# Performance work log

Hardware: AMD Instinct MI355X
Metric: run time of the kernel (lower is better)

## Reference

```python
import jax, jax.numpy as jnp
import numpy as np

HEADS = 16
DIM_HEAD = 64
QUERY_DIM = 1024
INNER_DIM = HEADS * DIM_HEAD  # 1024
SCALE = DIM_HEAD ** -0.5


def setup_inputs() -> dict:
    key = jax.random.key(0)
    ks = jax.random.split(key, 6)
    B, S = 2, 2048
    hidden_states = jax.random.normal(ks[0], (B, S, QUERY_DIM), dtype=jnp.float32)
    # torch Linear weights are [out, in]; store transposed [in, out] for x @ W
    w_q = jax.random.normal(ks[1], (QUERY_DIM, INNER_DIM), dtype=jnp.float32) * (QUERY_DIM ** -0.5)
    w_k = jax.random.normal(ks[2], (QUERY_DIM, INNER_DIM), dtype=jnp.float32) * (QUERY_DIM ** -0.5)
    w_v = jax.random.normal(ks[3], (QUERY_DIM, INNER_DIM), dtype=jnp.float32) * (QUERY_DIM ** -0.5)
    w_o = jax.random.normal(ks[4], (INNER_DIM, QUERY_DIM), dtype=jnp.float32) * (INNER_DIM ** -0.5)
    b_o = jax.random.normal(ks[5], (QUERY_DIM,), dtype=jnp.float32) * 0.01
    return {"hidden_states": hidden_states, "w_q": w_q, "w_k": w_k, "w_v": w_v, "w_o": w_o, "b_o": b_o}


def reference(hidden_states, w_q, w_k, w_v, w_o, b_o):
    B, S, _ = hidden_states.shape
    # QKV projections (context = hidden_states, i.e. self-attention)
    q = (hidden_states @ w_q).reshape(B, S, HEADS, DIM_HEAD)
    k = (hidden_states @ w_k).reshape(B, S, HEADS, DIM_HEAD)
    v = (hidden_states @ w_v).reshape(B, S, HEADS, DIM_HEAD)
    # scaled dot-product attention; scores materialized as [B, H, S, S]
    scores = jnp.einsum("bqhd,bkhd->bhqk", q, k) * SCALE
    probs = jax.nn.softmax(scores, axis=-1)
    out = jnp.einsum("bhqk,bkhd->bqhd", probs, v).reshape(B, S, INNER_DIM)
    return out @ w_o + b_o
```

## Files before the change

### kernel.cpp

```cpp
#include <hip/hip_runtime.h>
#include <cstdint>
#include <cstddef>

typedef unsigned short u16;
typedef unsigned int u32;
typedef __bf16 bf16x8 __attribute__((ext_vector_type(8)));
typedef float f32x4 __attribute__((ext_vector_type(4)));
typedef float f32x16 __attribute__((ext_vector_type(16)));
typedef u32 u32x2 __attribute__((ext_vector_type(2)));
typedef u32 u32x4 __attribute__((ext_vector_type(4)));

#define AS1 __attribute__((address_space(1)))
#define AS3 __attribute__((address_space(3)))

__device__ __forceinline__ void gld16(const u16* g, u16* l) {
  __builtin_amdgcn_global_load_lds((const AS1 void*)(const void*)g,
                                   (AS3 void*)(void*)l, 16, 0, 0);
}

__device__ __forceinline__ u16 f2bf(float f) {
  union { float f; unsigned u; } x; x.f = f;
  return (u16)((x.u + 0x7fffu + ((x.u >> 16) & 1u)) >> 16);
}

__device__ __forceinline__ float bf2f(u16 u) {
  union { u32 i; float f; } x; x.i = ((u32)u) << 16; return x.f;
}

__device__ __forceinline__ float fexp2(float x) {
  float r; asm("v_exp_f32 %0, %1" : "=v"(r) : "v"(x)); return r;
}

__device__ __forceinline__ f32x16 zf16() {
  f32x16 v;
#pragma unroll
  for (int i = 0; i < 16; ++i) v[i] = 0.f;
  return v;
}

__device__ __forceinline__ bf16x8 mk8(u32x2 a, u32x2 b) {
  union { u32x4 u; bf16x8 v; } x;
  x.u[0] = a[0]; x.u[1] = a[1]; x.u[2] = b[0]; x.u[3] = b[1];
  return x.v;
}

__global__ void k_prep(const float* __restrict__ X,
                       const float* __restrict__ wq, const float* __restrict__ wk,
                       const float* __restrict__ wv, const float* __restrict__ wo,
                       u16* __restrict__ Xb, u16* __restrict__ Wqkv, u16* __restrict__ Wot) {
  const int z = blockIdx.z;
  if (z == 4) {
    int bid = blockIdx.y * 32 + blockIdx.x;
    int tid = threadIdx.y * 32 + threadIdx.x;
#pragma unroll
    for (int k = 0; k < 4; ++k) {
      int i = bid * 1024 + k * 256 + tid;
      float4 v = reinterpret_cast<const float4*>(X)[i];
      ushort4 o;
      o.x = f2bf(v.x); o.y = f2bf(v.y); o.z = f2bf(v.z); o.w = f2bf(v.w);
      reinterpret_cast<ushort4*>(Xb)[i] = o;
    }
    return;
  }
  __shared__ float t[32][33];
  const float* in = (z == 0) ? wq : (z == 1) ? wk : (z == 2) ? wv : wo;
  u16* out = (z < 3) ? (Wqkv + (size_t)z * 1048576) : Wot;
  int bx = blockIdx.x * 32, by = blockIdx.y * 32;
  int tx = threadIdx.x, ty = threadIdx.y;
#pragma unroll
  for (int j = 0; j < 32; j += 8)
    t[ty + j][tx] = in[(size_t)(by + ty + j) * 1024 + bx + tx];
  __syncthreads();
#pragma unroll
  for (int j = 0; j < 32; j += 8)
    out[(size_t)(bx + ty + j) * 1024 + by + tx] = f2bf(t[tx][ty + j]);
}

__global__ __launch_bounds__(256) void k_gemm_qkv(
    const u16* __restrict__ Xb,
    const u16* __restrict__ Wt,
    u16* __restrict__ Qb,
    u16* __restrict__ Kb,
    u16* __restrict__ Vt) {
  __shared__ __align__(16) u16 As[128][32];
  __shared__ __align__(16) u16 Bs[128][32];
  const int tid = threadIdx.x;
  const int w = tid >> 6, l = tid & 63;
  const int bm = blockIdx.x * 128;
  const int bn = blockIdx.y * 128;
  const int wm = (w >> 1) * 64, wn = (w & 1) * 64;
  const int lm = l & 15, lg = l >> 4;

  f32x4 acc[4][4];
#pragma unroll
  for (int i = 0; i < 4; ++i)
#pragma unroll
    for (int j = 0; j < 4; ++j) acc[i][j] = f32x4{0.f, 0.f, 0.f, 0.f};

  const int srow = w * 16 + (l >> 2);
  const int scol = (l & 3) * 8;
  for (int k0 = 0; k0 < 1024; k0 += 32) {
#pragma unroll
    for (int j = 0; j < 2; ++j) {
      gld16(Xb + (size_t)(bm + j * 64 + srow) * 1024 + k0 + scol, &As[j * 64 + w * 16][0]);
      gld16(Wt + (size_t)(bn + j * 64 + srow) * 1024 + k0 + scol, &Bs[j * 64 + w * 16][0]);
    }
    __syncthreads();
    bf16x8 af[4], bfr[4];
#pragma unroll
    for (int mt = 0; mt < 4; ++mt)
      af[mt] = *reinterpret_cast<const bf16x8*>(&As[wm + mt * 16 + lm][lg * 8]);
#pragma unroll
    for (int nt = 0; nt < 4; ++nt)
      bfr[nt] = *reinterpret_cast<const bf16x8*>(&Bs[wn + nt * 16 + lm][lg * 8]);
#pragma unroll
    for (int mt = 0; mt < 4; ++mt)
#pragma unroll
      for (int nt = 0; nt < 4; ++nt)
        acc[mt][nt] = __builtin_amdgcn_mfma_f32_16x16x32_bf16(af[mt], bfr[nt], acc[mt][nt], 0, 0, 0);
    __syncthreads();
  }
#pragma unroll
  for (int nt = 0; nt < 4; ++nt) {
    int gc = bn + wn + nt * 16 + lm;
    int which = gc >> 10, jc = gc & 1023, h = jc >> 6, d = jc & 63;
#pragma unroll
    for (int mt = 0; mt < 4; ++mt) {
#pragma unroll
      for (int r = 0; r < 4; ++r) {
        int gr = bm + wm + mt * 16 + lg * 4 + r;
        int b = gr >> 11, s = gr & 2047;
        float v = acc[mt][nt][r];
        size_t bh = (size_t)(b * 16 + h);
        if (which == 0)      Qb[(bh * 2048 + s) * 64 + d] = f2bf(v * 0.18033688f);
        else if (which == 1) Kb[(bh * 2048 + s) * 64 + d] = f2bf(v);
        else                 Vt[(bh * 64 + d) * 2048 + s] = f2bf(v);
      }
    }
  }
}

__global__ __launch_bounds__(256) void k_attn(
    const u16* __restrict__ Qb, const u16* __restrict__ Kb,
    const u16* __restrict__ Vt,
    u16* __restrict__ Opb,
    float* __restrict__ lsums) {
  __shared__ __align__(16) u16 Ks[2][4224];
  __shared__ __align__(16) u16 Vs[2][4224];
  const int tid = threadIdx.x, w = tid >> 6, l = tid & 63;
  const int lm = l & 31, hi = l >> 5;
  const int kx = lm & 7;
  const int bh = blockIdx.x;
  const int q0 = blockIdx.y * 128 + w * 32;
  const int z = blockIdx.z;
  const u16* Qh = Qb + (size_t)bh * 2048 * 64;
  const u16* Kh = Kb + ((size_t)bh * 2048 + z * 1024) * 64;
  const u16* Vh = Vt + (size_t)bh * 64 * 2048 + z * 1024;

  bf16x8 qf[4];
#pragma unroll
  for (int c = 0; c < 4; ++c)
    qf[c] = *reinterpret_cast<const bf16x8*>(&Qh[(size_t)(q0 + lm) * 64 + 16 * c + 8 * hi]);

  f32x16 o0 = zf16(), o1 = zf16();
  float lsum = 0.f;

  const int sr8 = l >> 3;
  const int sg = l & 7;
  const int koff = (lm >> 3) * 528 + (lm & 7) * 64;

#define STAGE(tile, buf)                                                          \
  {                                                                               \
    const int kvn_ = (tile) * 64;                                                 \
    _Pragma("unroll")                                                             \
    for (int j = 0; j < 2; ++j) {                                                 \
      int row_ = w * 16 + j * 8 + sr8;                                            \
      int g_ = sg ^ sr8;                                                          \
      gld16(Kh + (size_t)(kvn_ + row_) * 64 + 8 * g_, &Ks[buf][(w * 2 + j) * 528]); \
      gld16(Vh + (size_t)row_ * 2048 + kvn_ + 8 * g_, &Vs[buf][(w * 2 + j) * 528]); \
    }                                                                             \
  }

  STAGE(0, 0);
  __syncthreads();

  for (int t = 0; t < 16; ++t) {
    const int cur = t & 1, nxt = cur ^ 1;

    if (t < 15) STAGE(t + 1, nxt);

    const u16* Kc = &Ks[cur][0];
    bf16x8 pf[2][2];
    float ps0 = 0.f, ps1 = 0.f, ps2 = 0.f, ps3 = 0.f;

    {
      f32x16 st = zf16();
      __builtin_amdgcn_s_setprio(1);
#pragma unroll
      for (int c = 0; c < 4; ++c) {
        bf16x8 kf = *reinterpret_cast<const bf16x8*>(Kc + koff + 8 * ((2 * c + hi) ^ kx));
        st = __builtin_amdgcn_mfma_f32_32x32x16_bf16(kf, qf[c], st, 0, 0, 0);
      }
      __builtin_amdgcn_s_setprio(0);
#pragma unroll
      for (int j = 0; j < 2; ++j)
#pragma unroll
        for (int ii = 0; ii < 8; ++ii) {
          float p = fexp2(st[8 * j + ii]);
          pf[0][j][ii] = (__bf16)p;
          if ((ii & 3) == 0)      ps0 += p;
          else if ((ii & 3) == 1) ps1 += p;
          else if ((ii & 3) == 2) ps2 += p;
          else                    ps3 += p;
        }
    }
    {
      f32x16 st = zf16();
      __builtin_amdgcn_s_setprio(1);
#pragma unroll
      for (int c = 0; c < 4; ++c) {
        bf16x8 kf = *reinterpret_cast<const bf16x8*>(Kc + koff + 2112 + 8 * ((2 * c + hi) ^ kx));
        st = __builtin_amdgcn_mfma_f32_32x32x16_bf16(kf, qf[c], st, 0, 0, 0);
      }
      __builtin_amdgcn_s_setprio(0);
#pragma unroll
      for (int j = 0; j < 2; ++j)
#pragma unroll
        for (int ii = 0; ii < 8; ++ii) {
          float p = fexp2(st[8 * j + ii]);
          pf[1][j][ii] = (__bf16)p;
          if ((ii & 3) == 0)      ps0 += p;
          else if ((ii & 3) == 1) ps1 += p;
          else if ((ii & 3) == 2) ps2 += p;
          else                    ps3 += p;
        }
    }
    float ps = (ps0 + ps1) + (ps2 + ps3);
    ps += __shfl_xor(ps, 32);
    lsum += ps;

    const u16* Vc = &Vs[cur][0];
    __builtin_amdgcn_s_setprio(1);
#pragma unroll
    for (int tt = 0; tt < 2; ++tt)
#pragma unroll
      for (int j = 0; j < 2; ++j) {
        int Ga = 4 * tt + 2 * j;
        u32x2 a0 = *reinterpret_cast<const u32x2*>(Vc + koff + 8 * (Ga ^ kx) + 4 * hi);
        u32x2 a1 = *reinterpret_cast<const u32x2*>(Vc + koff + 8 * ((Ga + 1) ^ kx) + 4 * hi);
        u32x2 b0 = *reinterpret_cast<const u32x2*>(Vc + koff + 2112 + 8 * (Ga ^ kx) + 4 * hi);
        u32x2 b1 = *reinterpret_cast<const u32x2*>(Vc + koff + 2112 + 8 * ((Ga + 1) ^ kx) + 4 * hi);
        o0 = __builtin_amdgcn_mfma_f32_32x32x16_bf16(pf[tt][j], mk8(a0, a1), o0, 0, 0, 0);
        o1 = __builtin_amdgcn_mfma_f32_32x32x16_bf16(pf[tt][j], mk8(b0, b1), o1, 0, 0, 0);
      }
    __builtin_amdgcn_s_setprio(0);

    __syncthreads();
  }
#undef STAGE

  const size_t robase = ((size_t)z * 32 + bh) * 2048 + q0;
  if (!hi) lsums[robase + lm] = lsum;
#pragma unroll
  for (int r = 0; r < 16; ++r) {
    int cr = (r & 3) + 8 * (r >> 2) + 4 * hi;
    size_t ro = (robase + cr) * 64;
    Opb[ro + lm]      = f2bf(o0[r]);
    Opb[ro + 32 + lm] = f2bf(o1[r]);
  }
}

__global__ __launch_bounds__(256) void k_merge(
    const u16* __restrict__ Opb, const float* __restrict__ lsums,
    u16* __restrict__ Ab) {
  int idx = blockIdx.x * 256 + threadIdx.x;
  int d8 = idx & 7, q = (idx >> 3) & 2047, bh = idx >> 14;
  size_t r0 = (size_t)bh * 2048 + q;
  size_t r1 = (size_t)(32 + bh) * 2048 + q;
  float inv = 1.0f / (lsums[r0] + lsums[r1]);
  u32x4 a0 = *reinterpret_cast<const u32x4*>(&Opb[r0 * 64 + d8 * 8]);
  u32x4 a1 = *reinterpret_cast<const u32x4*>(&Opb[r1 * 64 + d8 * 8]);
  u32x4 o;
#pragma unroll
  for (int j = 0; j < 4; ++j) {
    float lo = (bf2f((u16)(a0[j] & 0xffff)) + bf2f((u16)(a1[j] & 0xffff))) * inv;
    float hb = (bf2f((u16)(a0[j] >> 16))    + bf2f((u16)(a1[j] >> 16)))    * inv;
    o[j] = (u32)f2bf(lo) | ((u32)f2bf(hb) << 16);
  }
  int b = bh >> 4, h = bh & 15;
  *reinterpret_cast<u32x4*>(&Ab[((size_t)b * 2048 + q) * 1024 + h * 64 + d8 * 8]) = o;
}

__global__ __launch_bounds__(256) void k_gemm_out(
    const u16* __restrict__ Ab,
    const u16* __restrict__ Wot,
    const float* __restrict__ bias, float* __restrict__ out) {
  __shared__ __align__(16) u16 As[128][32];
  __shared__ __align__(16) u16 Bs[128][32];
  const int tid = threadIdx.x;
  const int w = tid >> 6, l = tid & 63;
  const int bm = blockIdx.x * 128;
  const int bn = blockIdx.y * 128;
  const int wm = (w >> 1) * 64, wn = (w & 1) * 64;
  const int lm = l & 15, lg = l >> 4;

  f32x4 acc[4][4];
#pragma unroll
  for (int i = 0; i < 4; ++i)
#pragma unroll
    for (int j = 0; j < 4; ++j) acc[i][j] = f32x4{0.f, 0.f, 0.f, 0.f};

  const int srow = w * 16 + (l >> 2);
  const int scol = (l & 3) * 8;
  for (int k0 = 0; k0 < 1024; k0 += 32) {
#pragma unroll
    for (int j = 0; j < 2; ++j) {
      gld16(Ab  + (size_t)(bm + j * 64 + srow) * 1024 + k0 + scol, &As[j * 64 + w * 16][0]);
      gld16(Wot + (size_t)(bn + j * 64 + srow) * 1024 + k0 + scol, &Bs[j * 64 + w * 16][0]);
    }
    __syncthreads();
    bf16x8 af[4], bfr[4];
#pragma unroll
    for (int mt = 0; mt < 4; ++mt)
      af[mt] = *reinterpret_cast<const bf16x8*>(&As[wm + mt * 16 + lm][lg * 8]);
#pragma unroll
    for (int nt = 0; nt < 4; ++nt)
      bfr[nt] = *reinterpret_cast<const bf16x8*>(&Bs[wn + nt * 16 + lm][lg * 8]);
#pragma unroll
    for (int mt = 0; mt < 4; ++mt)
#pragma unroll
      for (int nt = 0; nt < 4; ++nt)
        acc[mt][nt] = __builtin_amdgcn_mfma_f32_16x16x32_bf16(af[mt], bfr[nt], acc[mt][nt], 0, 0, 0);
    __syncthreads();
  }
#pragma unroll
  for (int nt = 0; nt < 4; ++nt) {
    int gc = bn + wn + nt * 16 + lm;
    float bv = bias[gc];
#pragma unroll
    for (int mt = 0; mt < 4; ++mt) {
#pragma unroll
      for (int r = 0; r < 4; ++r) {
        int gr = bm + wm + mt * 16 + lg * 4 + r;
        out[(size_t)gr * 1024 + gc] = acc[mt][nt][r] + bv;
      }
    }
  }
}

extern "C" void kernel_launch(void* const* d_in, const int* in_sizes, int n_in,
                              void* d_out, int out_size, void* d_ws, size_t ws_size,
                              hipStream_t stream) {
  const float* X  = (const float*)d_in[0];
  const float* wq = (const float*)d_in[1];
  const float* wk = (const float*)d_in[2];
  const float* wv = (const float*)d_in[3];
  const float* wo = (const float*)d_in[4];
  const float* bo = (const float*)d_in[5];
  float* out = (float*)d_out;

  char* ws = (char*)d_ws;
  u16*   Xb    = (u16*)(ws);
  u16*   Wqkv  = (u16*)(ws + (size_t)(8u  << 20));
  u16*   Wot   = (u16*)(ws + (size_t)(14u << 20));
  u16*   Qb    = (u16*)(ws + (size_t)(16u << 20));
  u16*   Kb    = (u16*)(ws + (size_t)(24u << 20));
  u16*   Vt    = (u16*)(ws + (size_t)(32u << 20));
  u16*   Opb   = (u16*)(ws + (size_t)(40u << 20));
  float* lsums = (float*)(ws + (size_t)(8u << 20));
  u16*   Ab    = (u16*)(ws);

  k_prep<<<dim3(32, 32, 5), dim3(32, 8), 0, stream>>>(X, wq, wk, wv, wo, Xb, Wqkv, Wot);
  k_gemm_qkv<<<dim3(32, 24), 256, 0, stream>>>(Xb, Wqkv, Qb, Kb, Vt);
  k_attn<<<dim3(32, 16, 2), 256, 0, stream>>>(Qb, Kb, Vt, Opb, lsums);
  k_merge<<<2048, 256, 0, stream>>>(Opb, lsums, Ab);
  k_gemm_out<<<dim3(32, 8), 256, 0, stream>>>(Ab, Wot, bo, out);
}
```

Baseline: 128.7 us.

## Process 64 query rows per wave in attention to reuse K/V fragments

Each wave now handles two 32-row query blocks, so every K and V fragment read from LDS feeds two MFMAs, and the grid's query dimension is halved. LDS is changed from the padded 528-stride layout to an unpadded 64x64 layout that relies only on an XOR swizzle. The row-sum shuffle moves out of the loop to the end. This doubles accumulator and probability register use and halves the block count (512 blocks), which may lower occupancy and latency hiding.

```diff
diff --git a/kernel.cpp b/kernel.cpp
--- a/kernel.cpp
+++ b/kernel.cpp
@@ -145,40 +145,41 @@
     const u16* __restrict__ Vt,
     u16* __restrict__ Opb,
     float* __restrict__ lsums) {
-  __shared__ __align__(16) u16 Ks[2][4224];
-  __shared__ __align__(16) u16 Vs[2][4224];
+  __shared__ __align__(16) u16 Ks[2][64][64];
+  __shared__ __align__(16) u16 Vs[2][64][64];
   const int tid = threadIdx.x, w = tid >> 6, l = tid & 63;
   const int lm = l & 31, hi = l >> 5;
   const int kx = lm & 7;
   const int bh = blockIdx.x;
-  const int q0 = blockIdx.y * 128 + w * 32;
+  const int q0 = blockIdx.y * 256 + w * 64;
   const int z = blockIdx.z;
   const u16* Qh = Qb + (size_t)bh * 2048 * 64;
   const u16* Kh = Kb + ((size_t)bh * 2048 + z * 1024) * 64;
   const u16* Vh = Vt + (size_t)bh * 64 * 2048 + z * 1024;
 
-  bf16x8 qf[4];
-#pragma unroll
-  for (int c = 0; c < 4; ++c)
-    qf[c] = *reinterpret_cast<const bf16x8*>(&Qh[(size_t)(q0 + lm) * 64 + 16 * c + 8 * hi]);
-
-  f32x16 o0 = zf16(), o1 = zf16();
-  float lsum = 0.f;
+  bf16x8 qA[4], qB[4];
+#pragma unroll
+  for (int c = 0; c < 4; ++c) {
+    qA[c] = *reinterpret_cast<const bf16x8*>(&Qh[(size_t)(q0 + lm) * 64 + 16 * c + 8 * hi]);
+    qB[c] = *reinterpret_cast<const bf16x8*>(&Qh[(size_t)(q0 + 32 + lm) * 64 + 16 * c + 8 * hi]);
+  }
+
+  f32x16 o00 = zf16(), o01 = zf16(), o10 = zf16(), o11 = zf16();
+  float ls0 = 0.f, ls1 = 0.f;
 
   const int sr8 = l >> 3;
   const int sg = l & 7;
-  const int koff = (lm >> 3) * 528 + (lm & 7) * 64;
-
-#define STAGE(tile, buf)                                                          \
-  {                                                                               \
-    const int kvn_ = (tile) * 64;                                                 \
-    _Pragma("unroll")                                                             \
-    for (int j = 0; j < 2; ++j) {                                                 \
-      int row_ = w * 16 + j * 8 + sr8;                                            \
-      int g_ = sg ^ sr8;                                                          \
-      gld16(Kh + (size_t)(kvn_ + row_) * 64 + 8 * g_, &Ks[buf][(w * 2 + j) * 528]); \
-      gld16(Vh + (size_t)row_ * 2048 + kvn_ + 8 * g_, &Vs[buf][(w * 2 + j) * 528]); \
-    }                                                                             \
+
+#define STAGE(tile, buf)                                                        \
+  {                                                                             \
+    const int kvn_ = (tile) * 64;                                               \
+    _Pragma("unroll")                                                           \
+    for (int j = 0; j < 2; ++j) {                                               \
+      int row_ = w * 16 + j * 8 + sr8;                                          \
+      int g_ = sg ^ (row_ & 7);                                                 \
+      gld16(Kh + (size_t)(kvn_ + row_) * 64 + 8 * g_, &Ks[buf][w * 16 + j * 8][0]); \
+      gld16(Vh + (size_t)row_ * 2048 + kvn_ + 8 * g_, &Vs[buf][w * 16 + j * 8][0]); \
+    }                                                                           \
   }
 
   STAGE(0, 0);
@@ -189,69 +190,72 @@
 
     if (t < 15) STAGE(t + 1, nxt);
 
-    const u16* Kc = &Ks[cur][0];
-    bf16x8 pf[2][2];
-    float ps0 = 0.f, ps1 = 0.f, ps2 = 0.f, ps3 = 0.f;
+    const u16* Kc = &Ks[cur][0][0];
+    bf16x8 pA[2][2], pB[2][2];
 
     {
-      f32x16 st = zf16();
+      f32x16 sa = zf16(), sb = zf16();
       __builtin_amdgcn_s_setprio(1);
 #pragma unroll
       for (int c = 0; c < 4; ++c) {
-        bf16x8 kf = *reinterpret_cast<const bf16x8*>(Kc + koff + 8 * ((2 * c + hi) ^ kx));
-        st = __builtin_amdgcn_mfma_f32_32x32x16_bf16(kf, qf[c], st, 0, 0, 0);
+        bf16x8 kf = *reinterpret_cast<const bf16x8*>(Kc + (size_t)lm * 64 + 8 * ((2 * c + hi) ^ kx));
+        sa = __builtin_amdgcn_mfma_f32_32x32x16_bf16(kf, qA[c], sa, 0, 0, 0);
+        sb = __builtin_amdgcn_mfma_f32_32x32x16_bf16(kf, qB[c], sb, 0, 0, 0);
       }
       __builtin_amdgcn_s_setprio(0);
+      float pa0 = 0.f, pa1 = 0.f, pb0 = 0.f, pb1 = 0.f;
 #pragma unroll
       for (int j = 0; j < 2; ++j)
 #pragma unroll
         for (int ii = 0; ii < 8; ++ii) {
-          float p = fexp2(st[8 * j + ii]);
-          pf[0][j][ii] = (__bf16)p;
-          if ((ii & 3) == 0)      ps0 += p;
-          else if ((ii & 3) == 1) ps1 += p;
-          else if ((ii & 3) == 2) ps2 += p;
-          else                    ps3 += p;
+          float pa = fexp2(sa[8 * j + ii]);
+          float pb = fexp2(sb[8 * j + ii]);
+          pA[0][j][ii] = (__bf16)pa;
+          pB[0][j][ii] = (__bf16)pb;
+          if (ii & 1) { pa1 += pa; pb1 += pb; } else { pa0 += pa; pb0 += pb; }
         }
+      ls0 += pa0 + pa1; ls1 += pb0 + pb1;
     }
     {
-      f32x16 st = zf16();
+      f32x16 sa = zf16(), sb = zf16();
       __builtin_amdgcn_s_setprio(1);
 #pragma unroll
       for (int c = 0; c < 4; ++c) {
-        bf16x8 kf = *reinterpret_cast<const bf16x8*>(Kc + koff + 2112 + 8 * ((2 * c + hi) ^ kx));
-        st = __builtin_amdgcn_mfma_f32_32x32x16_bf16(kf, qf[c], st, 0, 0, 0);
+        bf16x8 kf = *reinterpret_cast<const bf16x8*>(Kc + (size_t)(32 + lm) * 64 + 8 * ((2 * c + hi) ^ kx));
+        sa = __builtin_amdgcn_mfma_f32_32x32x16_bf16(kf, qA[c], sa, 0, 0, 0);
+        sb = __builtin_amdgcn_mfma_f32_32x32x16_bf16(kf, qB[c], sb, 0, 0, 0);
       }
       __builtin_amdgcn_s_setprio(0);
+      float pa0 = 0.f, pa1 = 0.f, pb0 = 0.f, pb1 = 0.f;
 #pragma unroll
       for (int j = 0; j < 2; ++j)
 #pragma unroll
         for (int ii = 0; ii < 8; ++ii) {
-          float p = fexp2(st[8 * j + ii]);
-          pf[1][j][ii] = (__bf16)p;
-          if ((ii & 3) == 0)      ps0 += p;
-          else if ((ii & 3) == 1) ps1 += p;
-          else if ((ii & 3) == 2) ps2 += p;
-          else                    ps3 += p;
+          float pa = fexp2(sa[8 * j + ii]);
+          float pb = fexp2(sb[8 * j + ii]);
+          pA[1][j][ii] = (__bf16)pa;
+          pB[1][j][ii] = (__bf16)pb;
+          if (ii & 1) { pa1 += pa; pb1 += pb; } else { pa0 += pa; pb0 += pb; }
         }
-    }
-    float ps = (ps0 + ps1) + (ps2 + ps3);
-    ps += __shfl_xor(ps, 32);
-    lsum += ps;
-
-    const u16* Vc = &Vs[cur][0];
+      ls0 += pa0 + pa1; ls1 += pb0 + pb1;
+    }
+
+    const u16* Vc = &Vs[cur][0][0];
     __builtin_amdgcn_s_setprio(1);
 #pragma unroll
     for (int tt = 0; tt < 2; ++tt)
 #pragma unroll
       for (int j = 0; j < 2; ++j) {
         int Ga = 4 * tt + 2 * j;
-        u32x2 a0 = *reinterpret_cast<const u32x2*>(Vc + koff + 8 * (Ga ^ kx) + 4 * hi);
-        u32x2 a1 = *reinterpret_cast<const u32x2*>(Vc + koff + 8 * ((Ga + 1) ^ kx) + 4 * hi);
-        u32x2 b0 = *reinterpret_cast<const u32x2*>(Vc + koff + 2112 + 8 * (Ga ^ kx) + 4 * hi);
-        u32x2 b1 = *reinterpret_cast<const u32x2*>(Vc + koff + 2112 + 8 * ((Ga + 1) ^ kx) + 4 * hi);
-        o0 = __builtin_amdgcn_mfma_f32_32x32x16_bf16(pf[tt][j], mk8(a0, a1), o0, 0, 0, 0);
-        o1 = __builtin_amdgcn_mfma_f32_32x32x16_bf16(pf[tt][j], mk8(b0, b1), o1, 0, 0, 0);
+        u32x2 a0 = *reinterpret_cast<const u32x2*>(Vc + (size_t)lm * 64 + 8 * (Ga ^ kx) + 4 * hi);
+        u32x2 a1 = *reinterpret_cast<const u32x2*>(Vc + (size_t)lm * 64 + 8 * ((Ga + 1) ^ kx) + 4 * hi);
+        u32x2 b0 = *reinterpret_cast<const u32x2*>(Vc + (size_t)(32 + lm) * 64 + 8 * (Ga ^ kx) + 4 * hi);
+        u32x2 b1 = *reinterpret_cast<const u32x2*>(Vc + (size_t)(32 + lm) * 64 + 8 * ((Ga + 1) ^ kx) + 4 * hi);
+        bf16x8 va = mk8(a0, a1), vb = mk8(b0, b1);
+        o00 = __builtin_amdgcn_mfma_f32_32x32x16_bf16(pA[tt][j], va, o00, 0, 0, 0);
+        o01 = __builtin_amdgcn_mfma_f32_32x32x16_bf16(pA[tt][j], vb, o01, 0, 0, 0);
+        o10 = __builtin_amdgcn_mfma_f32_32x32x16_bf16(pB[tt][j], va, o10, 0, 0, 0);
+        o11 = __builtin_amdgcn_mfma_f32_32x32x16_bf16(pB[tt][j], vb, o11, 0, 0, 0);
       }
     __builtin_amdgcn_s_setprio(0);
 
@@ -259,14 +263,22 @@
   }
 #undef STAGE
 
+  ls0 += __shfl_xor(ls0, 32);
+  ls1 += __shfl_xor(ls1, 32);
   const size_t robase = ((size_t)z * 32 + bh) * 2048 + q0;
-  if (!hi) lsums[robase + lm] = lsum;
+  if (!hi) {
+    lsums[robase + lm] = ls0;
+    lsums[robase + 32 + lm] = ls1;
+  }
 #pragma unroll
   for (int r = 0; r < 16; ++r) {
     int cr = (r & 3) + 8 * (r >> 2) + 4 * hi;
     size_t ro = (robase + cr) * 64;
-    Opb[ro + lm]      = f2bf(o0[r]);
-    Opb[ro + 32 + lm] = f2bf(o1[r]);
+    Opb[ro + lm]      = f2bf(o00[r]);
+    Opb[ro + 32 + lm] = f2bf(o01[r]);
+    size_t ro2 = (robase + 32 + cr) * 64;
+    Opb[ro2 + lm]      = f2bf(o10[r]);
+    Opb[ro2 + 32 + lm] = f2bf(o11[r]);
   }
 }
 
@@ -372,7 +384,7 @@
 
   k_prep<<<dim3(32, 32, 5), dim3(32, 8), 0, stream>>>(X, wq, wk, wv, wo, Xb, Wqkv, Wot);
   k_gemm_qkv<<<dim3(32, 24), 256, 0, stream>>>(Xb, Wqkv, Qb, Kb, Vt);
-  k_attn<<<dim3(32, 16, 2), 256, 0, stream>>>(Qb, Kb, Vt, Opb, lsums);
+  k_attn<<<dim3(32, 8, 2), 256, 0, stream>>>(Qb, Kb, Vt, Opb, lsums);
   k_merge<<<2048, 256, 0, stream>>>(Opb, lsums, Ab);
   k_gemm_out<<<dim3(32, 8), 256, 0, stream>>>(Ab, Wot, bo, out);
 }
```

Result: slower. 137.8 us (+7.1%).
